# Performance work log

Hardware: AMD Instinct MI355X
Metric: run time of the kernel (lower is better)

Reference implementation:

```python
import jax, jax.numpy as jnp
import numpy as np

G = 9.80665  # scipy.constants.g


def _xavier(key, fan_in, fan_out):
    std = np.sqrt(2.0 / (fan_in + fan_out))
    return jax.random.normal(key, (fan_in, fan_out), dtype=jnp.float32) * std


def setup_inputs() -> dict:
    key = jax.random.key(0)
    ks = jax.random.split(key, 16)
    n_samples, n_nodes, n_pipes, n_demand, hidden = 16384, 512, 1024, 256, 64
    D = jax.random.uniform(ks[0], (n_samples, n_demand), dtype=jnp.float32) * 0.01
    leak_id = jax.random.randint(ks[1], (n_samples, 1), 0, n_pipes)
    A0 = jax.random.normal(ks[2], (n_nodes, n_pipes), dtype=jnp.float32) * 0.1
    inv = jax.random.normal(ks[3], (n_nodes, n_pipes), dtype=jnp.float32) * 0.1
    M = jax.random.normal(ks[4], (n_nodes, n_pipes), dtype=jnp.float32) * 0.1
    supply = jax.random.uniform(ks[5], (n_pipes,), dtype=jnp.float32) * 10.0
    L = jax.random.uniform(ks[6], (n_pipes,), dtype=jnp.float32) * 900.0 + 100.0  # pipe length [m]
    d = jax.random.uniform(ks[7], (n_pipes,), dtype=jnp.float32) * 0.4 + 0.1      # diameter [m]
    C = jax.random.uniform(ks[8], (n_pipes,), dtype=jnp.float32) * 50.0 + 100.0   # HW coefficient
    demand_idx = jnp.arange(n_demand) * 2  # distinct node indices < n_nodes
    a = jnp.float32(0.01)   # leak area
    Cd = jnp.float32(0.75)  # discharge coefficient
    W1 = _xavier(ks[9], 1, hidden); b1 = jnp.zeros((hidden,), jnp.float32)
    W2 = _xavier(ks[10], hidden, hidden); b2 = jnp.zeros((hidden,), jnp.float32)
    W3 = _xavier(ks[11], hidden, 1); b3 = jnp.zeros((1,), jnp.float32)
    base = jax.random.normal(ks[12], (n_pipes,), dtype=jnp.float32) * 0.1
    return {"D": D, "leak_id": leak_id, "A0": A0, "inv": inv, "M": M,
            "supply": supply, "L": L, "d": d, "C": C, "a": a, "Cd": Cd,
            "W1": W1, "b1": b1, "W2": W2, "b2": b2, "W3": W3, "b3": b3,
            "base": base, "demand_idx": demand_idx}


def reference(D, leak_id, A0, inv, M, supply, L, d, C, a, Cd,
              W1, b1, W2, b2, W3, b3, base, demand_idx):
    S = D.shape[0]
    n_nodes, n_pipes = M.shape
    idx = leak_id[:, 0]  # [S] int, pipe index per sample

    # Net(leak_id): tanh MLP + lookup of per-pipe base value
    x = leak_id.astype(jnp.float32)                      # [S,1]
    h = jnp.tanh(x @ W1 + b1)
    h = jnp.tanh(h @ W2 + b2)
    net_out = base[idx][:, None] + (h @ W3 + b3)          # [S,1]

    # scatter-built demand / leakage / areas
    demand = jnp.zeros((S, n_nodes), jnp.float32).at[:, demand_idx].set(D)
    rows = jnp.arange(S)
    leakage = jnp.zeros((S, n_pipes), jnp.float32).at[rows, idx].set(net_out[:, 0])
    areas = jnp.zeros((S, n_pipes), jnp.float32).at[rows, idx].set(a)

    # q = inv.T @ (M @ leakage + demand)
    y = jnp.einsum('np,sp->sn', M, leakage) + demand      # [S,Nn]
    q = jnp.einsum('np,sn->sp', inv, y)                   # [S,Np]

    # Hazen-Williams head loss
    hL = jnp.sign(q) * 10.667 * C[None] ** (-1.852) * d[None] ** (-4.871) * L[None] * jnp.abs(q) ** 1.852
    H = jnp.einsum('np,sp->sn', inv, supply[None] - hL)   # [S,Nn]

    # leak demand d_leak = Cd * (M @ areas) * sqrt(2 g relu(H))  (safe sqrt)
    Hp = jax.nn.relu(H)
    sq = jnp.sqrt(jnp.where(Hp > 0, Hp, 1.0)) * (Hp > 0).astype(jnp.float32)
    d_leak = Cd * jnp.einsum('np,sp->sn', M, areas) * jnp.sqrt(jnp.float32(2.0 * G)) * sq

    residual = jnp.einsum('np,sp->sn', A0, q) - demand - d_leak
    return jnp.mean(residual ** 2)
```

## Files before the change

kernel.cpp:

```cpp
#include <hip/hip_runtime.h>
#include <math.h>

typedef _Float16 f16;
typedef _Float16 f16x4 __attribute__((ext_vector_type(4)));
typedef _Float16 f16x8 __attribute__((ext_vector_type(8)));
typedef float f32x4 __attribute__((ext_vector_type(4)));

#define S_TOTAL 16384
#define N_NODES 512
#define N_PIPES 1024
#define N_DEM   256
#define HIDDEN  64
#define T_SCALE 256.0f

#define GLOAD16(gsrc, ldst) \
    __builtin_amdgcn_global_load_lds((const __attribute__((address_space(1))) void*)(gsrc), \
                                     (__attribute__((address_space(3))) void*)(ldst), 16, 0, 0)
#define SBAR()  __builtin_amdgcn_s_barrier()
#define FENCE() asm volatile("" ::: "memory")
#define WAITN(n) asm volatile("s_waitcnt vmcnt(" #n ")" ::: "memory")

__device__ __forceinline__ unsigned char f32_to_bf8(float x) {
    unsigned short h = __builtin_bit_cast(unsigned short, (f16)x);
    unsigned short r = (unsigned short)(h + 0x7F + ((h >> 8) & 1));
    return (unsigned char)(r >> 8);
}

__global__ __launch_bounds__(256) void prep_all(
    const float* __restrict__ W1, const float* __restrict__ b1,
    const float* __restrict__ W2, const float* __restrict__ b2,
    const float* __restrict__ W3, const float* __restrict__ b3,
    const float* __restrict__ base,
    const float* __restrict__ L, const float* __restrict__ dpipe,
    const float* __restrict__ Cw,
    const float* __restrict__ Mf, const float* __restrict__ inv,
    const float* __restrict__ A0, const float* __restrict__ D,
    const int* __restrict__ dmap,
    float* __restrict__ net, float* __restrict__ lKc,
    f16* __restrict__ MT16, f16* __restrict__ invT16,
    f16* __restrict__ inv16, unsigned char* __restrict__ inv8,
    f16* __restrict__ A016, unsigned char* __restrict__ D8,
    f16* __restrict__ DI16, unsigned char* __restrict__ IDXT8,
    float* __restrict__ out, int out_size)
{
    __shared__ __align__(16) f16 tile[64][72];
    const int b = blockIdx.x, t = threadIdx.x;
    if (b < 256) {
        if (b == 0) for (int i = t; i < out_size; i += 256) out[i] = 0.f;
        const int wid = t >> 6, k = t & 63;
        const int p = b * 4 + wid;
        const float x = (float)p;
        float h1 = tanhf(x * W1[k] + b1[k]);
        float acc = b2[k];
        #pragma unroll
        for (int j = 0; j < HIDDEN; ++j) {
            float hj = __shfl(h1, j, 64);
            acc = fmaf(hj, W2[j * HIDDEN + k], acc);
        }
        float partial = tanhf(acc) * W3[k];
        #pragma unroll
        for (int off = 32; off > 0; off >>= 1) partial += __shfl_down(partial, off, 64);
        if (k == 0) {
            net[p] = base[p] + partial + b3[0];
            lKc[p] = log2f(10.667f) - 1.852f * log2f(Cw[p]) - 4.871f * log2f(dpipe[p]) + log2f(L[p]);
        }
        return;
    }
    if (b < 512) {
        const int idx = b - 256;
        const float* in = (idx < 128) ? Mf : inv;
        f16* outp = (idx < 128) ? MT16 : invT16;
        const int i2 = idx & 127;
        const int bx = i2 & 15, by = i2 >> 4;
        const int r0 = by * 64, c0 = bx * 64;
        const int lr = t / 16, lc4 = (t % 16) * 4;
        #pragma unroll
        for (int i = 0; i < 4; ++i) {
            int r = lr + i * 16;
            float4 v = *(const float4*)(in + (size_t)(r0 + r) * N_PIPES + c0 + lc4);
            tile[lc4 + 0][r] = (f16)v.x; tile[lc4 + 1][r] = (f16)v.y;
            tile[lc4 + 2][r] = (f16)v.z; tile[lc4 + 3][r] = (f16)v.w;
        }
        __syncthreads();
        const int wrow = t / 4, wc16 = (t % 4) * 16;
        *(f16x8*)(outp + (size_t)(c0 + wrow) * N_NODES + r0 + wc16)     = *(f16x8*)&tile[wrow][wc16];
        *(f16x8*)(outp + (size_t)(c0 + wrow) * N_NODES + r0 + wc16 + 8) = *(f16x8*)&tile[wrow][wc16 + 8];
        return;
    }
    const int tid = (b - 512) * 256 + t;
    const int np = 768 * 256;
    for (int i = tid; i < (N_NODES * N_PIPES) / 4; i += np) {
        float4 v = ((const float4*)inv)[i];
        ((f16x4*)inv16)[i] = (f16x4){(f16)v.x, (f16)v.y, (f16)v.z, (f16)v.w};
        uchar4 v8 = {f32_to_bf8(v.x), f32_to_bf8(v.y), f32_to_bf8(v.z), f32_to_bf8(v.w)};
        ((uchar4*)inv8)[i] = v8;
        float4 w = ((const float4*)A0)[i];
        ((f16x4*)A016)[i] = (f16x4){(f16)w.x, (f16)w.y, (f16)w.z, (f16)w.w};
    }
    for (int i = tid; i < (S_TOTAL * N_DEM) / 4; i += np) {
        float4 v = ((const float4*)D)[i];
        uchar4 o = {f32_to_bf8(v.x), f32_to_bf8(v.y), f32_to_bf8(v.z), f32_to_bf8(v.w)};
        ((uchar4*)D8)[i] = o;
    }
    for (int i = tid; i < N_DEM * (N_PIPES / 4); i += np) {
        int j = i >> 8, p0 = (i & 255) * 4;
        float4 v = *(const float4*)(inv + (size_t)dmap[j] * N_PIPES + p0);
        *(f16x4*)(DI16 + (size_t)j * N_PIPES + p0) = (f16x4){(f16)v.x, (f16)v.y, (f16)v.z, (f16)v.w};
    }
    for (int i = tid; i < N_PIPES * (N_DEM / 4); i += np) {
        int p = i >> 6, j0 = (i & 63) * 4;
        uchar4 o;
        #pragma unroll
        for (int u = 0; u < 4; ++u)
            o[u] = f32_to_bf8(inv[(size_t)dmap[j0 + u] * N_PIPES + p]);
        *(uchar4*)(IDXT8 + (size_t)p * N_DEM + j0) = o;
    }
}

struct GemmP {
    const f16* A; int lda;
    const f16* B; int ldb;
    f16* C; int ldc;
    int K;
    const int* dmap;
    int gx, gy;
    unsigned char* C8;
};

__device__ __forceinline__ void gemm_body(const GemmP& P, int bx, int by) {
    __shared__ __align__(16) f16 As[128][72], Bs[64][72];
    const int m0 = by * 128, c0 = bx * 64;
    const int t = threadIdx.x, lane = t & 63, wid = t >> 6;
    const int wr = wid >> 1, wc = wid & 1;
    const int cl = lane & 15, g = lane >> 4;
    const int tr = t >> 3, tc = (t & 7) * 8;
    f32x4 acc[4][2] = {};
    for (int k0 = 0; k0 < P.K; k0 += 64) {
        #pragma unroll
        for (int r = 0; r < 4; ++r) {
            int row = r * 32 + tr;
            *(f16x8*)&As[row][tc] = *(const f16x8*)(P.A + (size_t)(m0 + row) * P.lda + k0 + tc);
        }
        #pragma unroll
        for (int r = 0; r < 2; ++r) {
            int row = r * 32 + tr;
            *(f16x8*)&Bs[row][tc] = *(const f16x8*)(P.B + (size_t)(c0 + row) * P.ldb + k0 + tc);
        }
        __syncthreads();
        #pragma unroll
        for (int kk = 0; kk < 2; ++kk) {
            const int kb = kk * 32 + g * 8;
            f16x8 a[4], bfr[2];
            #pragma unroll
            for (int m = 0; m < 4; ++m) a[m] = *(const f16x8*)&As[wr * 64 + m * 16 + cl][kb];
            #pragma unroll
            for (int n = 0; n < 2; ++n) bfr[n] = *(const f16x8*)&Bs[wc * 32 + n * 16 + cl][kb];
            #pragma unroll
            for (int m = 0; m < 4; ++m)
                #pragma unroll
                for (int n = 0; n < 2; ++n)
                    acc[m][n] = __builtin_amdgcn_mfma_f32_16x16x32_f16(a[m], bfr[n], acc[m][n], 0, 0, 0);
        }
        __syncthreads();
    }
    #pragma unroll
    for (int m = 0; m < 4; ++m)
        #pragma unroll
        for (int reg = 0; reg < 4; ++reg) {
            const int row = m0 + wr * 64 + m * 16 + g * 4 + reg;
            #pragma unroll
            for (int n = 0; n < 2; ++n) {
                const int col = c0 + wc * 32 + n * 16 + cl;
                float v = acc[m][n][reg];
                if (P.dmap && P.dmap[col] == row) v -= 1.0f;
                if (P.C8) P.C8[(size_t)row * P.ldc + col] = f32_to_bf8(v);
                else      P.C [(size_t)row * P.ldc + col] = (f16)v;
            }
        }
}

__global__ __launch_bounds__(256) void gemm_small3(GemmP p0, GemmP p1, GemmP p2) {
    const GemmP& P = (blockIdx.z == 0) ? p0 : (blockIdx.z == 1) ? p1 : p2;
    if ((int)blockIdx.x >= P.gx || (int)blockIdx.y >= P.gy) return;
    gemm_body(P, blockIdx.x, blockIdx.y);
}

__global__ __launch_bounds__(512, 4) void gemm_qt_mfma(
    const unsigned char* __restrict__ D8, const int* __restrict__ leak_id,
    const unsigned char* __restrict__ IDXT8, const float* __restrict__ net,
    const f16* __restrict__ G16, const float* __restrict__ lKc,
    const float* __restrict__ supply, unsigned char* __restrict__ t8,
    const f16* __restrict__ MT16, const f16* __restrict__ Wt,
    f16* __restrict__ G2out)
{
    __shared__ __align__(16) unsigned char As[2][128 * 128];
    __shared__ __align__(16) unsigned char Bs[2][128 * 128];
    const int t = threadIdx.x, lane = t & 63, wid = t >> 6;

    if (blockIdx.y >= 128) {
        f16 (*A2)[72] = (f16(*)[72])&Bs[0][0];
        f16 (*B2)[72] = (f16(*)[72])&As[0][0];
        const int m0 = ((int)blockIdx.y - 128) * 128, c0 = blockIdx.x * 64;
        const int wr = wid >> 2, wc = wid & 3;
        const int cl = lane & 15, g = lane >> 4;
        f32x4 acc[4] = {};
        for (int k0 = 0; k0 < 512; k0 += 64) {
            {
                int r = t >> 2, c16 = (t & 3) * 16;
                *(f16x8*)&A2[r][c16]     = *(const f16x8*)(MT16 + (size_t)(m0 + r) * N_NODES + k0 + c16);
                *(f16x8*)&A2[r][c16 + 8] = *(const f16x8*)(MT16 + (size_t)(m0 + r) * N_NODES + k0 + c16 + 8);
                int r2 = t >> 3, c8 = (t & 7) * 8;
                *(f16x8*)&B2[r2][c8] = *(const f16x8*)(Wt + (size_t)(c0 + r2) * N_NODES + k0 + c8);
            }
            __syncthreads();
            #pragma unroll
            for (int kk = 0; kk < 2; ++kk) {
                const int kb = kk * 32 + g * 8;
                f16x8 b = *(const f16x8*)&B2[wc * 16 + cl][kb];
                #pragma unroll
                for (int m = 0; m < 4; ++m) {
                    f16x8 a = *(const f16x8*)&A2[wr * 64 + m * 16 + cl][kb];
                    acc[m] = __builtin_amdgcn_mfma_f32_16x16x32_f16(a, b, acc[m], 0, 0, 0);
                }
            }
            __syncthreads();
        }
        #pragma unroll
        for (int m = 0; m < 4; ++m)
            #pragma unroll
            for (int reg = 0; reg < 4; ++reg)
                G2out[(size_t)(m0 + wr * 64 + m * 16 + g * 4 + reg) * N_NODES + c0 + wc * 16 + cl] = (f16)acc[m][reg];
        return;
    }
    const int bid = blockIdx.y * 8 + blockIdx.x;
    const int w = (bid & 7) * 128 + (bid >> 3);
    const int bx = w & 7, by = w >> 3;
    const int p0 = bx * 128, sb = by * 128;
    const int wr = wid >> 2, wc = wid & 3;
    const int cl = lane & 15, g = lane >> 4;
    const int swrow = lane >> 3;
    const int swb = ((lane & 7) ^ swrow) * 16;

    const unsigned char* Abase = D8    + (size_t)(sb + swrow) * N_DEM + swb;
    const unsigned char* Bbase = IDXT8 + (size_t)(p0 + swrow) * N_DEM + swb;

    f32x4 acc[4][2] = {};
    auto stage = [&](int buf, int k0) {
        #pragma unroll
        for (int c = 0; c < 2; ++c) {
            int r0 = wid * 16 + c * 8;
            GLOAD16(Abase + (size_t)r0 * N_DEM + k0, &As[buf][r0 * 128]);
        }
        #pragma unroll
        for (int c = 0; c < 2; ++c) {
            int r0 = wid * 16 + c * 8;
            GLOAD16(Bbase + (size_t)r0 * N_DEM + k0, &Bs[buf][r0 * 128]);
        }
    };
    auto compute = [&](int buf) {
        #pragma unroll
        for (int ks = 0; ks < 4; ++ks) {
            const int bo = (ks * 32 + g * 8) ^ ((cl & 7) << 4);
            long long a[4], b[2];
            #pragma unroll
            for (int m = 0; m < 4; ++m)
                a[m] = *(const long long*)&As[buf][(wr * 64 + m * 16 + cl) * 128 + bo];
            #pragma unroll
            for (int n = 0; n < 2; ++n)
                b[n] = *(const long long*)&Bs[buf][(wc * 32 + n * 16 + cl) * 128 + bo];
            #pragma unroll
            for (int m = 0; m < 4; ++m)
                #pragma unroll
                for (int n = 0; n < 2; ++n)
                    acc[m][n] = __builtin_amdgcn_mfma_f32_16x16x32_bf8_bf8(a[m], b[n], acc[m][n], 0, 0, 0);
        }
    };

    stage(0, 0);
    stage(1, 128);
    WAITN(4); SBAR();
    compute(0);
    FENCE(); SBAR();
    WAITN(0); SBAR();
    compute(1);

    float lKc2[2], sup2[2]; int pcol[2];
    #pragma unroll
    for (int n = 0; n < 2; ++n) {
        pcol[n] = p0 + wc * 32 + n * 16 + cl;
        lKc2[n] = lKc[pcol[n]]; sup2[n] = supply[pcol[n]];
    }
    #pragma unroll
    for (int m = 0; m < 4; ++m) {
        #pragma unroll
        for (int reg = 0; reg < 4; ++reg) {
            const int srow = sb + wr * 64 + m * 16 + g * 4 + reg;
            const int idx = leak_id[srow];
            const float nv = net[idx];
            #pragma unroll
            for (int n = 0; n < 2; ++n) {
                float qv = acc[m][n][reg] + nv * (float)G16[(size_t)idx * N_PIPES + pcol[n]];
                float l = __builtin_amdgcn_logf(fabsf(qv));
                float hL = copysignf(__builtin_amdgcn_exp2f(fmaf(1.852f, l, lKc2[n])), qv);
                t8[(size_t)srow * N_PIPES + pcol[n]] = f32_to_bf8((sup2[n] - hL) * (1.0f / T_SCALE));
            }
        }
    }
}

__global__ __launch_bounds__(512, 4) void gemm_res_mfma(
    const unsigned char* __restrict__ t8, const unsigned char* __restrict__ inv8,
    const unsigned char* __restrict__ D8, const unsigned char* __restrict__ P1p8,
    const f16* __restrict__ MT16, const f16* __restrict__ G2_16,
    const int* __restrict__ leak_id, const float* __restrict__ net,
    const float* __restrict__ Cd_p, const float* __restrict__ a_p,
    float scale, float* __restrict__ out)
{
    __shared__ __align__(16) unsigned char AsM[2][128 * 128];
    __shared__ __align__(16) unsigned char BsM[2][128 * 128];
    const int nwg = gridDim.x * gridDim.y;
    const int bid = blockIdx.y * gridDim.x + blockIdx.x;
    const int w = (bid & 7) * (nwg >> 3) + (bid >> 3);
    const int bx = w % gridDim.x, by = w / gridDim.x;
    const int n0 = bx * 128, sb = by * 128;
    const int t = threadIdx.x, lane = t & 63, wid = t >> 6;
    const int wr = wid >> 2, wc = wid & 3;
    const int cl = lane & 15, g = lane >> 4;
    const int swrow = lane >> 3;
    const int swb = ((lane & 7) ^ swrow) * 16;

    const unsigned char* HAb = t8   + (size_t)(sb + swrow) * N_PIPES + swb;
    const unsigned char* HBb = inv8 + (size_t)(n0 + swrow) * N_PIPES + swb;
    const unsigned char* RAb = D8   + (size_t)(sb + swrow) * N_DEM + swb;
    const unsigned char* RBb = P1p8 + (size_t)(n0 + swrow) * N_DEM + swb;

    f32x4 accH[4][2] = {}, accR[4][2] = {};

    auto stageH = [&](int buf, int k0) {
        #pragma unroll
        for (int c = 0; c < 2; ++c) {
            int r0 = wid * 16 + c * 8;
            GLOAD16(HAb + (size_t)r0 * N_PIPES + k0, &AsM[buf][r0 * 128]);
        }
        #pragma unroll
        for (int c = 0; c < 2; ++c) {
            int r0 = wid * 16 + c * 8;
            GLOAD16(HBb + (size_t)r0 * N_PIPES + k0, &BsM[buf][r0 * 128]);
        }
    };
    auto stageR = [&](int buf, int k0) {
        #pragma unroll
        for (int c = 0; c < 2; ++c) {
            int r0 = wid * 16 + c * 8;
            GLOAD16(RAb + (size_t)r0 * N_DEM + k0, &AsM[buf][r0 * 128]);
        }
        #pragma unroll
        for (int c = 0; c < 2; ++c) {
            int r0 = wid * 16 + c * 8;
            GLOAD16(RBb + (size_t)r0 * N_DEM + k0, &BsM[buf][r0 * 128]);
        }
    };
    auto computeT = [&](int buf, f32x4 (&accA)[4][2]) {
        #pragma unroll
        for (int ks = 0; ks < 4; ++ks) {
            const int bo = (ks * 32 + g * 8) ^ ((cl & 7) << 4);
            long long a[4], b[2];
            #pragma unroll
            for (int m = 0; m < 4; ++m)
                a[m] = *(const long long*)&AsM[buf][(wr * 64 + m * 16 + cl) * 128 + bo];
            #pragma unroll
            for (int n = 0; n < 2; ++n)
                b[n] = *(const long long*)&BsM[buf][(wc * 32 + n * 16 + cl) * 128 + bo];
            #pragma unroll
            for (int m = 0; m < 4; ++m)
                #pragma unroll
                for (int n = 0; n < 2; ++n)
                    accA[m][n] = __builtin_amdgcn_mfma_f32_16x16x32_bf8_bf8(a[m], b[n], accA[m][n], 0, 0, 0);
        }
    };

    int cur = 0;
    stageH(0, 0);
    #pragma unroll 1
    for (int k = 0; k < 7; ++k) {
        stageH(cur ^ 1, (k + 1) * 128);
        WAITN(4); SBAR();
        computeT(cur, accH);
        FENCE(); SBAR();
        cur ^= 1;
    }
    stageR(cur ^ 1, 0);
    WAITN(4); SBAR();
    computeT(cur, accH);
    FENCE(); SBAR();
    cur ^= 1;
    stageR(cur ^ 1, 128);
    WAITN(4); SBAR();
    computeT(cur, accR);
    FENCE(); SBAR();
    cur ^= 1;
    WAITN(0); SBAR();
    computeT(cur, accR);

    const float cda = Cd_p[0] * a_p[0] * sqrtf(2.f * 9.80665f);
    int node[2];
    #pragma unroll
    for (int n = 0; n < 2; ++n) node[n] = n0 + wc * 32 + n * 16 + cl;
    float lsum = 0.f;
    #pragma unroll
    for (int m = 0; m < 4; ++m) {
        #pragma unroll
        for (int reg = 0; reg < 4; ++reg) {
            const int srow = sb + wr * 64 + m * 16 + g * 4 + reg;
            const int idx = leak_id[srow];
            const float nv = net[idx];
            #pragma unroll
            for (int n = 0; n < 2; ++n) {
                const float H = accH[m][n][reg] * T_SCALE;
                const float sq = (H > 0.f) ? sqrtf(H) : 0.f;
                const float dl = cda * (float)MT16[(size_t)idx * N_NODES + node[n]] * sq;
                const float r = accR[m][n][reg] + nv * (float)G2_16[(size_t)idx * N_NODES + node[n]] - dl;
                lsum += r * r;
            }
        }
    }
    #pragma unroll
    for (int off = 32; off > 0; off >>= 1) lsum += __shfl_down(lsum, off, 64);
    __syncthreads();
    float* wred = (float*)&AsM[0][0];
    if (lane == 0) wred[wid] = lsum;
    __syncthreads();
    if (t == 0) {
        float tot = 0.f;
        #pragma unroll
        for (int i = 0; i < 8; ++i) tot += wred[i];
        atomicAdd(out, tot * scale);
    }
}

extern "C" void kernel_launch(void* const* d_in, const int* in_sizes, int n_in,
                              void* d_out, int out_size, void* d_ws, size_t ws_size,
                              hipStream_t stream) {
    const float* D          = (const float*)d_in[0];
    const int*   leak_id    = (const int*)  d_in[1];
    const float* A0         = (const float*)d_in[2];
    const float* inv        = (const float*)d_in[3];
    const float* M          = (const float*)d_in[4];
    const float* supply     = (const float*)d_in[5];
    const float* L          = (const float*)d_in[6];
    const float* dpipe      = (const float*)d_in[7];
    const float* C          = (const float*)d_in[8];
    const float* a_p        = (const float*)d_in[9];
    const float* Cd_p       = (const float*)d_in[10];
    const float* W1         = (const float*)d_in[11];
    const float* b1         = (const float*)d_in[12];
    const float* W2         = (const float*)d_in[13];
    const float* b2         = (const float*)d_in[14];
    const float* W3         = (const float*)d_in[15];
    const float* b3         = (const float*)d_in[16];
    const float* base       = (const float*)d_in[17];
    const int*   demand_idx = (const int*)  d_in[18];

    char* ws = (char*)d_ws;
    size_t off = 0;
    auto carve = [&](size_t bytes) { char* p = ws + off; off += (bytes + 255) & ~(size_t)255; return p; };
    float* net    = (float*)carve(N_PIPES * 4);
    float* lKc    = (float*)carve(N_PIPES * 4);
    f16* inv16  = (f16*)carve((size_t)N_NODES * N_PIPES * 2);
    unsigned char* inv8 = (unsigned char*)carve((size_t)N_NODES * N_PIPES);
    f16* A016   = (f16*)carve((size_t)N_NODES * N_PIPES * 2);
    f16* MT16   = (f16*)carve((size_t)N_PIPES * N_NODES * 2);
    f16* invT16 = (f16*)carve((size_t)N_PIPES * N_NODES * 2);
    f16* G16    = (f16*)carve((size_t)N_PIPES * N_PIPES * 2);
    f16* G2_16  = (f16*)carve((size_t)N_PIPES * N_NODES * 2);
    f16* Wt     = (f16*)carve((size_t)N_NODES * N_NODES * 2);
    unsigned char* P1p8 = (unsigned char*)carve((size_t)N_NODES * N_DEM);
    f16* DI16   = (f16*)carve((size_t)N_DEM * N_PIPES * 2);
    unsigned char* IDXT8 = (unsigned char*)carve((size_t)N_PIPES * N_DEM);
    unsigned char* D8    = (unsigned char*)carve((size_t)S_TOTAL * N_DEM);
    unsigned char* t8    = (unsigned char*)carve((size_t)S_TOTAL * N_PIPES);

    prep_all<<<1280, 256, 0, stream>>>(
        W1, b1, W2, b2, W3, b3, base, L, dpipe, C,
        M, inv, A0, D, demand_idx,
        net, lKc, MT16, invT16, inv16, inv8, A016, D8, DI16, IDXT8,
        (float*)d_out, out_size);

    GemmP pG16 = {MT16, N_NODES, invT16, N_NODES, G16, N_PIPES, N_NODES, nullptr, 16, 8, nullptr};
    GemmP pWt  = {A016, N_PIPES, inv16, N_PIPES, Wt, N_NODES, N_PIPES, nullptr, 8, 4, nullptr};
    GemmP pP1  = {A016, N_PIPES, DI16, N_PIPES, nullptr, N_DEM, N_PIPES, demand_idx, 4, 4, P1p8};
    gemm_small3<<<dim3(16, 8, 3), 256, 0, stream>>>(pG16, pWt, pP1);

    gemm_qt_mfma<<<dim3(8, 136), 512, 0, stream>>>(
        D8, leak_id, IDXT8, net, G16, lKc, supply, t8, MT16, Wt, G2_16);

    const float scale = 1.f / ((float)S_TOTAL * (float)N_NODES);
    gemm_res_mfma<<<dim3(N_NODES / 128, S_TOTAL / 128), 512, 0, stream>>>(
        t8, inv8, D8, P1p8, MT16, G2_16, leak_id, net, Cd_p, a_p,
        scale, (float*)d_out);
}
```

Before: 84.51 us.

## Fold small GEMMs into prep and main kernels, dropping the gemm_small3 launch

```diff
diff --git a/kernel.cpp b/kernel.cpp
--- a/kernel.cpp
+++ b/kernel.cpp
@@ -37,13 +37,14 @@
     const float* __restrict__ A0, const float* __restrict__ D,
     const int* __restrict__ dmap,
     float* __restrict__ net, float* __restrict__ lKc,
-    f16* __restrict__ MT16, f16* __restrict__ invT16,
-    f16* __restrict__ inv16, unsigned char* __restrict__ inv8,
+    f16* __restrict__ MT16, unsigned char* __restrict__ inv8,
     f16* __restrict__ A016, unsigned char* __restrict__ D8,
     f16* __restrict__ DI16, unsigned char* __restrict__ IDXT8,
+    f16* __restrict__ G16,
     float* __restrict__ out, int out_size)
 {
-    __shared__ __align__(16) f16 tile[64][72];
+    __shared__ __align__(16) f16 GAs[128][72];
+    __shared__ __align__(16) f16 GBs[64][72];
     const int b = blockIdx.x, t = threadIdx.x;
     if (b < 256) {
         if (b == 0) for (int i = t; i < out_size; i += 256) out[i] = 0.f;
@@ -66,123 +67,104 @@
         }
         return;
     }
-    if (b < 512) {
-        const int idx = b - 256;
-        const float* in = (idx < 128) ? Mf : inv;
-        f16* outp = (idx < 128) ? MT16 : invT16;
-        const int i2 = idx & 127;
+    if (b < 384) {
+        f16 (*tile)[72] = GBs;
+        const int i2 = b - 256;
         const int bx = i2 & 15, by = i2 >> 4;
         const int r0 = by * 64, c0 = bx * 64;
         const int lr = t / 16, lc4 = (t % 16) * 4;
         #pragma unroll
         for (int i = 0; i < 4; ++i) {
             int r = lr + i * 16;
-            float4 v = *(const float4*)(in + (size_t)(r0 + r) * N_PIPES + c0 + lc4);
+            float4 v = *(const float4*)(Mf + (size_t)(r0 + r) * N_PIPES + c0 + lc4);
             tile[lc4 + 0][r] = (f16)v.x; tile[lc4 + 1][r] = (f16)v.y;
             tile[lc4 + 2][r] = (f16)v.z; tile[lc4 + 3][r] = (f16)v.w;
         }
         __syncthreads();
         const int wrow = t / 4, wc16 = (t % 4) * 16;
-        *(f16x8*)(outp + (size_t)(c0 + wrow) * N_NODES + r0 + wc16)     = *(f16x8*)&tile[wrow][wc16];
-        *(f16x8*)(outp + (size_t)(c0 + wrow) * N_NODES + r0 + wc16 + 8) = *(f16x8*)&tile[wrow][wc16 + 8];
+        *(f16x8*)(MT16 + (size_t)(c0 + wrow) * N_NODES + r0 + wc16)     = *(f16x8*)&tile[wrow][wc16];
+        *(f16x8*)(MT16 + (size_t)(c0 + wrow) * N_NODES + r0 + wc16 + 8) = *(f16x8*)&tile[wrow][wc16 + 8];
         return;
     }
-    const int tid = (b - 512) * 256 + t;
-    const int np = 768 * 256;
-    for (int i = tid; i < (N_NODES * N_PIPES) / 4; i += np) {
-        float4 v = ((const float4*)inv)[i];
-        ((f16x4*)inv16)[i] = (f16x4){(f16)v.x, (f16)v.y, (f16)v.z, (f16)v.w};
-        uchar4 v8 = {f32_to_bf8(v.x), f32_to_bf8(v.y), f32_to_bf8(v.z), f32_to_bf8(v.w)};
-        ((uchar4*)inv8)[i] = v8;
-        float4 w = ((const float4*)A0)[i];
-        ((f16x4*)A016)[i] = (f16x4){(f16)w.x, (f16)w.y, (f16)w.z, (f16)w.w};
-    }
-    for (int i = tid; i < (S_TOTAL * N_DEM) / 4; i += np) {
-        float4 v = ((const float4*)D)[i];
-        uchar4 o = {f32_to_bf8(v.x), f32_to_bf8(v.y), f32_to_bf8(v.z), f32_to_bf8(v.w)};
-        ((uchar4*)D8)[i] = o;
-    }
-    for (int i = tid; i < N_DEM * (N_PIPES / 4); i += np) {
-        int j = i >> 8, p0 = (i & 255) * 4;
-        float4 v = *(const float4*)(inv + (size_t)dmap[j] * N_PIPES + p0);
-        *(f16x4*)(DI16 + (size_t)j * N_PIPES + p0) = (f16x4){(f16)v.x, (f16)v.y, (f16)v.z, (f16)v.w};
-    }
-    for (int i = tid; i < N_PIPES * (N_DEM / 4); i += np) {
-        int p = i >> 6, j0 = (i & 63) * 4;
-        uchar4 o;
-        #pragma unroll
-        for (int u = 0; u < 4; ++u)
-            o[u] = f32_to_bf8(inv[(size_t)dmap[j0 + u] * N_PIPES + p]);
-        *(uchar4*)(IDXT8 + (size_t)p * N_DEM + j0) = o;
-    }
-}
-
-struct GemmP {
-    const f16* A; int lda;
-    const f16* B; int ldb;
-    f16* C; int ldc;
-    int K;
-    const int* dmap;
-    int gx, gy;
-    unsigned char* C8;
-};
-
-__device__ __forceinline__ void gemm_body(const GemmP& P, int bx, int by) {
-    __shared__ __align__(16) f16 As[128][72], Bs[64][72];
-    const int m0 = by * 128, c0 = bx * 64;
-    const int t = threadIdx.x, lane = t & 63, wid = t >> 6;
-    const int wr = wid >> 1, wc = wid & 1;
-    const int cl = lane & 15, g = lane >> 4;
-    const int tr = t >> 3, tc = (t & 7) * 8;
-    f32x4 acc[4][2] = {};
-    for (int k0 = 0; k0 < P.K; k0 += 64) {
-        #pragma unroll
-        for (int r = 0; r < 4; ++r) {
-            int row = r * 32 + tr;
-            *(f16x8*)&As[row][tc] = *(const f16x8*)(P.A + (size_t)(m0 + row) * P.lda + k0 + tc);
-        }
-        #pragma unroll
-        for (int r = 0; r < 2; ++r) {
-            int row = r * 32 + tr;
-            *(f16x8*)&Bs[row][tc] = *(const f16x8*)(P.B + (size_t)(c0 + row) * P.ldb + k0 + tc);
-        }
-        __syncthreads();
-        #pragma unroll
-        for (int kk = 0; kk < 2; ++kk) {
-            const int kb = kk * 32 + g * 8;
-            f16x8 a[4], bfr[2];
-            #pragma unroll
-            for (int m = 0; m < 4; ++m) a[m] = *(const f16x8*)&As[wr * 64 + m * 16 + cl][kb];
-            #pragma unroll
-            for (int n = 0; n < 2; ++n) bfr[n] = *(const f16x8*)&Bs[wc * 32 + n * 16 + cl][kb];
-            #pragma unroll
-            for (int m = 0; m < 4; ++m)
+    if (b < 1152) {
+        const int tid = (b - 384) * 256 + t;
+        const int np = 768 * 256;
+        for (int i = tid; i < (N_NODES * N_PIPES) / 4; i += np) {
+            float4 v = ((const float4*)inv)[i];
+            uchar4 v8 = {f32_to_bf8(v.x), f32_to_bf8(v.y), f32_to_bf8(v.z), f32_to_bf8(v.w)};
+            ((uchar4*)inv8)[i] = v8;
+            float4 w = ((const float4*)A0)[i];
+            ((f16x4*)A016)[i] = (f16x4){(f16)w.x, (f16)w.y, (f16)w.z, (f16)w.w};
+        }
+        for (int i = tid; i < (S_TOTAL * N_DEM) / 4; i += np) {
+            float4 v = ((const float4*)D)[i];
+            uchar4 o = {f32_to_bf8(v.x), f32_to_bf8(v.y), f32_to_bf8(v.z), f32_to_bf8(v.w)};
+            ((uchar4*)D8)[i] = o;
+        }
+        for (int i = tid; i < N_DEM * (N_PIPES / 4); i += np) {
+            int j = i >> 8, p0 = (i & 255) * 4;
+            float4 v = *(const float4*)(inv + (size_t)dmap[j] * N_PIPES + p0);
+            *(f16x4*)(DI16 + (size_t)j * N_PIPES + p0) = (f16x4){(f16)v.x, (f16)v.y, (f16)v.z, (f16)v.w};
+        }
+        for (int i = tid; i < N_PIPES * (N_DEM / 4); i += np) {
+            int p = i >> 6, j0 = (i & 63) * 4;
+            uchar4 o;
+            #pragma unroll
+            for (int u = 0; u < 4; ++u)
+                o[u] = f32_to_bf8(inv[(size_t)dmap[j0 + u] * N_PIPES + p]);
+            *(uchar4*)(IDXT8 + (size_t)p * N_DEM + j0) = o;
+        }
+        return;
+    }
+    {
+        const int bb = b - 1152;
+        const int i0 = (bb >> 4) * 128, p0 = (bb & 15) * 64;
+        const int lane = t & 63, wid = t >> 6;
+        const int wr = wid >> 1, wc = wid & 1;
+        const int cl = lane & 15, g = lane >> 4;
+        f32x4 acc[4][2] = {};
+        for (int n0 = 0; n0 < N_NODES; n0 += 64) {
+            #pragma unroll
+            for (int pass = 0; pass < 8; ++pass) {
+                int k = pass * 8 + (t >> 5), c4 = (t & 31) * 4;
+                float4 v = *(const float4*)(Mf + (size_t)(n0 + k) * N_PIPES + i0 + c4);
+                GAs[c4 + 0][k] = (f16)v.x; GAs[c4 + 1][k] = (f16)v.y;
+                GAs[c4 + 2][k] = (f16)v.z; GAs[c4 + 3][k] = (f16)v.w;
+            }
+            #pragma unroll
+            for (int pass = 0; pass < 4; ++pass) {
+                int k = pass * 16 + (t >> 4), c4 = (t & 15) * 4;
+                float4 w = *(const float4*)(inv + (size_t)(n0 + k) * N_PIPES + p0 + c4);
+                GBs[c4 + 0][k] = (f16)w.x; GBs[c4 + 1][k] = (f16)w.y;
+                GBs[c4 + 2][k] = (f16)w.z; GBs[c4 + 3][k] = (f16)w.w;
+            }
+            __syncthreads();
+            #pragma unroll
+            for (int kk = 0; kk < 2; ++kk) {
+                const int kb = kk * 32 + g * 8;
+                f16x8 a[4], bfr[2];
+                #pragma unroll
+                for (int m = 0; m < 4; ++m) a[m] = *(const f16x8*)&GAs[wr * 64 + m * 16 + cl][kb];
+                #pragma unroll
+                for (int n = 0; n < 2; ++n) bfr[n] = *(const f16x8*)&GBs[wc * 32 + n * 16 + cl][kb];
+                #pragma unroll
+                for (int m = 0; m < 4; ++m)
+                    #pragma unroll
+                    for (int n = 0; n < 2; ++n)
+                        acc[m][n] = __builtin_amdgcn_mfma_f32_16x16x32_f16(a[m], bfr[n], acc[m][n], 0, 0, 0);
+            }
+            __syncthreads();
+        }
+        #pragma unroll
+        for (int m = 0; m < 4; ++m)
+            #pragma unroll
+            for (int reg = 0; reg < 4; ++reg) {
+                const int row = i0 + wr * 64 + m * 16 + g * 4 + reg;
                 #pragma unroll
                 for (int n = 0; n < 2; ++n)
-                    acc[m][n] = __builtin_amdgcn_mfma_f32_16x16x32_f16(a[m], bfr[n], acc[m][n], 0, 0, 0);
-        }
-        __syncthreads();
-    }
-    #pragma unroll
-    for (int m = 0; m < 4; ++m)
-        #pragma unroll
-        for (int reg = 0; reg < 4; ++reg) {
-            const int row = m0 + wr * 64 + m * 16 + g * 4 + reg;
-            #pragma unroll
-            for (int n = 0; n < 2; ++n) {
-                const int col = c0 + wc * 32 + n * 16 + cl;
-                float v = acc[m][n][reg];
-                if (P.dmap && P.dmap[col] == row) v -= 1.0f;
-                if (P.C8) P.C8[(size_t)row * P.ldc + col] = f32_to_bf8(v);
-                else      P.C [(size_t)row * P.ldc + col] = (f16)v;
-            }
-        }
-}
-
-__global__ __launch_bounds__(256) void gemm_small3(GemmP p0, GemmP p1, GemmP p2) {
-    const GemmP& P = (blockIdx.z == 0) ? p0 : (blockIdx.z == 1) ? p1 : p2;
-    if ((int)blockIdx.x >= P.gx || (int)blockIdx.y >= P.gy) return;
-    gemm_body(P, blockIdx.x, blockIdx.y);
+                    G16[(size_t)row * N_PIPES + p0 + wc * 32 + n * 16 + cl] = (f16)acc[m][n][reg];
+            }
+    }
 }
 
 __global__ __launch_bounds__(512, 4) void gemm_qt_mfma(
@@ -190,27 +172,38 @@
     const unsigned char* __restrict__ IDXT8, const float* __restrict__ net,
     const f16* __restrict__ G16, const float* __restrict__ lKc,
     const float* __restrict__ supply, unsigned char* __restrict__ t8,
-    const f16* __restrict__ MT16, const f16* __restrict__ Wt,
-    f16* __restrict__ G2out)
+    const f16* __restrict__ A016, const f16* __restrict__ DI16,
+    f16* __restrict__ G2out, unsigned char* __restrict__ P1p8,
+    const int* __restrict__ dmap)
 {
     __shared__ __align__(16) unsigned char As[2][128 * 128];
     __shared__ __align__(16) unsigned char Bs[2][128 * 128];
     const int t = threadIdx.x, lane = t & 63, wid = t >> 6;
 
     if (blockIdx.y >= 128) {
+        const f16 *Ar, *Br; f16* Cf; unsigned char* C8; const int* dm;
+        int m0, ldc;
+        const int c0 = blockIdx.x * 64;
+        if (blockIdx.y < 136) {
+            m0 = ((int)blockIdx.y - 128) * 128;
+            Ar = G16; Br = A016; Cf = G2out; C8 = nullptr; dm = nullptr; ldc = N_NODES;
+        } else {
+            if ((int)blockIdx.x >= 4) return;
+            m0 = ((int)blockIdx.y - 136) * 128;
+            Ar = A016; Br = DI16; Cf = nullptr; C8 = P1p8; dm = dmap; ldc = N_DEM;
+        }
         f16 (*A2)[72] = (f16(*)[72])&Bs[0][0];
         f16 (*B2)[72] = (f16(*)[72])&As[0][0];
-        const int m0 = ((int)blockIdx.y - 128) * 128, c0 = blockIdx.x * 64;
         const int wr = wid >> 2, wc = wid & 3;
         const int cl = lane & 15, g = lane >> 4;
         f32x4 acc[4] = {};
-        for (int k0 = 0; k0 < 512; k0 += 64) {
+        for (int k0 = 0; k0 < 1024; k0 += 64) {
             {
                 int r = t >> 2, c16 = (t & 3) * 16;
-                *(f16x8*)&A2[r][c16]     = *(const f16x8*)(MT16 + (size_t)(m0 + r) * N_NODES + k0 + c16);
-                *(f16x8*)&A2[r][c16 + 8] = *(const f16x8*)(MT16 + (size_t)(m0 + r) * N_NODES + k0 + c16 + 8);
+                *(f16x8*)&A2[r][c16]     = *(const f16x8*)(Ar + (size_t)(m0 + r) * N_PIPES + k0 + c16);
+                *(f16x8*)&A2[r][c16 + 8] = *(const f16x8*)(Ar + (size_t)(m0 + r) * N_PIPES + k0 + c16 + 8);
                 int r2 = t >> 3, c8 = (t & 7) * 8;
-                *(f16x8*)&B2[r2][c8] = *(const f16x8*)(Wt + (size_t)(c0 + r2) * N_NODES + k0 + c8);
+                *(f16x8*)&B2[r2][c8] = *(const f16x8*)(Br + (size_t)(c0 + r2) * N_PIPES + k0 + c8);
             }
             __syncthreads();
             #pragma unroll
@@ -228,8 +221,14 @@
         #pragma unroll
         for (int m = 0; m < 4; ++m)
             #pragma unroll
-            for (int reg = 0; reg < 4; ++reg)
-                G2out[(size_t)(m0 + wr * 64 + m * 16 + g * 4 + reg) * N_NODES + c0 + wc * 16 + cl] = (f16)acc[m][reg];
+            for (int reg = 0; reg < 4; ++reg) {
+                const int row = m0 + wr * 64 + m * 16 + g * 4 + reg;
+                const int col = c0 + wc * 16 + cl;
+                float v = acc[m][reg];
+                if (dm && dm[col] == row) v -= 1.0f;
+                if (C8) C8[(size_t)row * ldc + col] = f32_to_bf8(v);
+                else    Cf[(size_t)row * ldc + col] = (f16)v;
+            }
         return;
     }
     const int bid = blockIdx.y * 8 + blockIdx.x;
@@ -466,14 +465,11 @@
     auto carve = [&](size_t bytes) { char* p = ws + off; off += (bytes + 255) & ~(size_t)255; return p; };
     float* net    = (float*)carve(N_PIPES * 4);
     float* lKc    = (float*)carve(N_PIPES * 4);
-    f16* inv16  = (f16*)carve((size_t)N_NODES * N_PIPES * 2);
     unsigned char* inv8 = (unsigned char*)carve((size_t)N_NODES * N_PIPES);
     f16* A016   = (f16*)carve((size_t)N_NODES * N_PIPES * 2);
     f16* MT16   = (f16*)carve((size_t)N_PIPES * N_NODES * 2);
-    f16* invT16 = (f16*)carve((size_t)N_PIPES * N_NODES * 2);
     f16* G16    = (f16*)carve((size_t)N_PIPES * N_PIPES * 2);
     f16* G2_16  = (f16*)carve((size_t)N_PIPES * N_NODES * 2);
-    f16* Wt     = (f16*)carve((size_t)N_NODES * N_NODES * 2);
     unsigned char* P1p8 = (unsigned char*)carve((size_t)N_NODES * N_DEM);
     f16* DI16   = (f16*)carve((size_t)N_DEM * N_PIPES * 2);
     unsigned char* IDXT8 = (unsigned char*)carve((size_t)N_PIPES * N_DEM);
@@ -483,16 +479,12 @@
     prep_all<<<1280, 256, 0, stream>>>(
         W1, b1, W2, b2, W3, b3, base, L, dpipe, C,
         M, inv, A0, D, demand_idx,
-        net, lKc, MT16, invT16, inv16, inv8, A016, D8, DI16, IDXT8,
+        net, lKc, MT16, inv8, A016, D8, DI16, IDXT8, G16,
         (float*)d_out, out_size);
 
-    GemmP pG16 = {MT16, N_NODES, invT16, N_NODES, G16, N_PIPES, N_NODES, nullptr, 16, 8, nullptr};
-    GemmP pWt  = {A016, N_PIPES, inv16, N_PIPES, Wt, N_NODES, N_PIPES, nullptr, 8, 4, nullptr};
-    GemmP pP1  = {A016, N_PIPES, DI16, N_PIPES, nullptr, N_DEM, N_PIPES, demand_idx, 4, 4, P1p8};
-    gemm_small3<<<dim3(16, 8, 3), 256, 0, stream>>>(pG16, pWt, pP1);
-
-    gemm_qt_mfma<<<dim3(8, 136), 512, 0, stream>>>(
-        D8, leak_id, IDXT8, net, G16, lKc, supply, t8, MT16, Wt, G2_16);
+    gemm_qt_mfma<<<dim3(8, 140), 512, 0, stream>>>(
+        D8, leak_id, IDXT8, net, G16, lKc, supply, t8,
+        A016, DI16, G2_16, P1p8, demand_idx);
 
     const float scale = 1.f / ((float)S_TOTAL * (float)N_NODES);
     gemm_res_mfma<<<dim3(N_NODES / 128, S_TOTAL / 128), 512, 0, stream>>>(
```

Measured after the change: 108.9 us. 1.29x slower.
